# Optimization experiments

Hardware: AMD Instinct MI355X
Metric: run time of the kernel (lower is better)

The kernel has to match this reference:

```python
import jax, jax.numpy as jnp
import numpy as np

SHAPES = ((100, 152), (50, 76), (25, 38), (13, 19))  # per-level (H, W), stride 8/16/32/64 of 800x1216
S_TOTAL = sum(h * w for h, w in SHAPES)  # 20197
D, H, LVL, P, NL, H2 = 256, 8, 4, 4, 6, 2
B, NQ_TOTAL, NPROP = 8, 350, 300
DFF = 1024


def layer_norm(x, w, b, eps=1e-5):
    m = jnp.mean(x, -1, keepdims=True)
    v = jnp.mean((x - m) ** 2, -1, keepdims=True)
    return (x - m) / jnp.sqrt(v + eps) * w + b


def pos2posemb(pos, num_pos_feats=64, temperature=10000.0):
    pos = pos * (2.0 * np.pi)
    dim_t = temperature ** (2.0 * (jnp.arange(num_pos_feats) // 2).astype(jnp.float32) / num_pos_feats)
    pe = pos[..., None] / dim_t  # [..., 4, 64]
    pe = jnp.stack((jnp.sin(pe[..., 0::2]), jnp.cos(pe[..., 1::2])), axis=-1)  # [..., 4, 32, 2]
    return pe.reshape(pe.shape[:-3] + (-1,))  # [..., 256]


def bilinear_gather(v_l, loc, hl, wl):
    # v_l [B, hl*wl, H, Dh]; loc [B, Nq, H, P, 2] in [0,1]; grid_sample align_corners=False, zero padding
    b, nq, h, p, _ = loc.shape
    dh = v_l.shape[-1]
    x = loc[..., 0] * wl - 0.5
    y = loc[..., 1] * hl - 0.5
    x0 = jnp.floor(x)
    y0 = jnp.floor(y)
    lx = x - x0
    ly = y - y0

    def g(xi, yi):
        valid = (xi >= 0) & (xi <= wl - 1) & (yi >= 0) & (yi <= hl - 1)
        xi_i = jnp.clip(xi, 0, wl - 1).astype(jnp.int32)
        yi_i = jnp.clip(yi, 0, hl - 1).astype(jnp.int32)
        idx = (yi_i * wl + xi_i).transpose(0, 1, 3, 2).reshape(b, nq * p, h)  # per-head spatial index
        out = jnp.take_along_axis(v_l, jnp.broadcast_to(idx[..., None], (b, nq * p, h, dh)), axis=1)
        out = out.reshape(b, nq, p, h, dh).transpose(0, 1, 3, 2, 4)  # [B,Nq,H,P,Dh]
        return out * valid.astype(v_l.dtype)[..., None]

    return (g(x0, y0) * ((1 - lx) * (1 - ly))[..., None]
            + g(x0 + 1, y0) * (lx * (1 - ly))[..., None]
            + g(x0, y0 + 1) * ((1 - lx) * ly)[..., None]
            + g(x0 + 1, y0 + 1) * (lx * ly)[..., None])


def ms_deform_attn(query, ref, src, Woff, boff, Wa, ba, Wv, bv, Wout, bout):
    b, nq, d = query.shape
    dh = d // H
    value = (src @ Wv + bv).reshape(b, -1, H, dh)
    off = (query @ Woff + boff).reshape(b, nq, H, LVL, P, 2)
    attn = jax.nn.softmax((query @ Wa + ba).reshape(b, nq, H, LVL * P), -1).reshape(b, nq, H, LVL, P)
    # 4-d reference points: center + offsets scaled by box size
    loc = ref[:, :, None, :, None, :2] + off / P * ref[:, :, None, :, None, 2:] * 0.5  # [b,nq,H,L,P,2]
    out = jnp.zeros((b, nq, H, dh), query.dtype)
    start = 0
    for l, (hl, wl) in enumerate(SHAPES):
        v_l = value[:, start:start + hl * wl]
        start += hl * wl
        samp = bilinear_gather(v_l, loc[:, :, :, l], hl, wl)  # [b,nq,H,P,dh]
        out = out + (samp * attn[:, :, :, l, :, None]).sum(3)
    return out.reshape(b, nq, d) @ Wout + bout


def weight_attn(q_in, k_in, Wq, bq, Wk, bk):
    b, nq, d = q_in.shape
    nk = k_in.shape[1]
    dh = d // H2
    q = (q_in @ Wq + bq).reshape(b, nq, H2, dh).transpose(0, 2, 1, 3)
    k = (k_in @ Wk + bk).reshape(b, nk, H2, dh).transpose(0, 2, 1, 3)
    mm = jax.nn.softmax(jnp.einsum('bhqd,bhkd->bhqk', q, k) * (1.0 / dh ** 0.5), -1)
    qn = q / (jnp.linalg.norm(q, axis=-1, keepdims=True) + 1e-6)
    kn = k / (jnp.linalg.norm(k, axis=-1, keepdims=True) + 1e-6)
    cos = jnp.einsum('bhqd,bhkd->bhqk', qn, kn)
    return cos, mm


def setup_inputs():
    key = jax.random.key(0)
    ks = jax.random.split(key, 32)
    f = jnp.float32
    inp = {}
    inp['tgt'] = jax.random.normal(ks[0], (B, NQ_TOTAL, D), f)
    inp['reference_points'] = jax.random.uniform(ks[1], (B, NQ_TOTAL, 4), f, 0.05, 0.95)
    inp['src'] = jax.random.normal(ks[2], (B, S_TOTAL, D), f)
    inp['src_spatial_shapes'] = jnp.array(SHAPES, jnp.int32)
    lsi = np.cumsum([0] + [h * w for h, w in SHAPES])[:-1]
    inp['src_level_start_index'] = jnp.array(lsi, jnp.int32)
    inp['src_valid_ratios'] = jnp.ones((B, LVL, 2), f)
    inp['num_proposals'] = NPROP
    names = [('Woff', (NL, D, H * LVL * P * 2)), ('boff', (NL, H * LVL * P * 2)),
             ('Wa', (NL, D, H * LVL * P)), ('ba', (NL, H * LVL * P)),
             ('Wv', (NL, D, D)), ('bv', (NL, D)), ('Wout', (NL, D, D)), ('bout', (NL, D)),
             ('Wl1', (NL, D, DFF)), ('bl1', (NL, DFF)), ('Wl2', (NL, DFF, D)), ('bl2', (NL, D)),
             ('Wq', (NL, D, D)), ('bq', (NL, D)), ('Wk', (NL, D, D)), ('bk', (NL, D))]
    for i, (n, s) in enumerate(names):
        inp[n] = jax.random.normal(ks[3 + i], s, f) * 0.02
    inp['n1w'] = jnp.ones((NL, D), f)
    inp['n1b'] = jnp.zeros((NL, D), f)
    inp['n3w'] = jnp.ones((NL, D), f)
    inp['n3b'] = jnp.zeros((NL, D), f)
    return inp


def reference(tgt, reference_points, src, src_spatial_shapes, src_level_start_index,
              src_valid_ratios, num_proposals, Woff, boff, Wa, ba, Wv, bv, Wout, bout,
              Wl1, bl1, Wl2, bl2, Wq, bq, Wk, bk, n1w, n1b, n3w, n3b):
    proposals = tgt[:, :num_proposals]
    track_queries = tgt[:, num_proposals:]
    p_ref = reference_points[:, :num_proposals]
    t_ref = reference_points[:, num_proposals:]
    vr = jnp.concatenate([src_valid_ratios, src_valid_ratios], -1)  # [B,L,4]
    ref_input = p_ref[:, :, None] * vr[:, None]  # [B,Np,L,4]
    p_pos = pos2posemb(p_ref)
    t_pos = pos2posemb(t_ref)  # computed per torch code; WeightAttention ignores pos
    for l in range(NL):
        q = proposals + p_pos
        ca = ms_deform_attn(q, ref_input, src, Woff[l], boff[l], Wa[l], ba[l], Wv[l], bv[l], Wout[l], bout[l])
        proposals = layer_norm(proposals + ca, n1w[l], n1b[l])  # dropout = identity (eval)
        ffn = jax.nn.relu(proposals @ Wl1[l] + bl1[l]) @ Wl2[l] + bl2[l]
        proposals = layer_norm(proposals + ffn, n3w[l], n3b[l])
        pt_cos, pt_mm = weight_attn(proposals, track_queries, Wq[l], bq[l], Wk[l], bk[l])
        pp_cos, pp_mm = weight_attn(proposals, proposals, Wq[l], bq[l], Wk[l], bk[l])
    return proposals, p_ref, pt_cos, pp_cos, pt_mm, pp_mm
```

## Files before the change

### kernel.cpp

```cpp
#include <hip/hip_runtime.h>

#define BB 8
#define NQ 300
#define NTQ 50
#define NLAY 6
#define S_TOTAL 20197
#define ROWS (BB*NQ)
#define MVAL (BB*S_TOTAL)

typedef unsigned short u16;
typedef unsigned int u32;
typedef __bf16 v8bf __attribute__((ext_vector_type(8)));
typedef float f32x4 __attribute__((ext_vector_type(4)));

__device__ __forceinline__ u16 f2b(float f) {
    u32 u = __float_as_uint(f);
    u32 r = (u + 0x7fffu + ((u >> 16) & 1u)) >> 16;
    return (u16)r;
}
__device__ __forceinline__ u32 pk2(float lo, float hi) {
    return (u32)f2b(lo) | ((u32)f2b(hi) << 16);
}

#define ASYNC_CP16(dst_lds, src_g) \
    __builtin_amdgcn_global_load_lds((const __attribute__((address_space(1))) u32*)(src_g), \
                                     (__attribute__((address_space(3))) u32*)(dst_lds), 16, 0, 0)

__global__ void transpose_pack(
    const float* Woff, const float* Wa, const float* Wv, const float* Wout,
    const float* Wl1, const float* Wl2, const float* Wq, const float* Wk,
    const float* boff, const float* ba, const float* bvp, const float* bout,
    const float* bl1, const float* bl2, const float* bq, const float* bk,
    u16* wt, float* bias)
{
    int idx = blockIdx.x * 256 + threadIdx.x;
    if (idx < 5308416) {
        int l = idx / 884736;
        int o = idx % 884736;
        float v;
        if (o < 98304) { int n = o >> 8, k = o & 255;
            v = (n < 256) ? Woff[l*65536 + k*256 + n] : Wa[l*32768 + k*128 + (n-256)];
        } else if (o < 163840) { int o2 = o - 98304; int n = o2 >> 8, k = o2 & 255;
            v = Wv[l*65536 + k*256 + n];
        } else if (o < 229376) { int o2 = o - 163840; int n = o2 >> 8, k = o2 & 255;
            v = Wout[l*65536 + k*256 + n];
        } else if (o < 491520) { int o2 = o - 229376; int n = o2 >> 8, k = o2 & 255;
            v = Wl1[l*262144 + k*1024 + n];
        } else if (o < 753664) { int o2 = o - 491520; int n = o2 >> 10, k = o2 & 1023;
            v = Wl2[l*262144 + k*256 + n];
        } else { int o2 = o - 753664; int n = o2 >> 8, k = o2 & 255;
            v = (n < 256) ? Wq[l*65536 + k*256 + n] : Wk[l*65536 + k*256 + (n-256)];
        }
        wt[idx] = f2b(v);
    } else {
        int i2 = idx - 5308416;
        if (i2 < 16128) {
            int l = i2 / 2688, o = i2 % 2688;
            float v;
            if (o < 256)       v = boff[l*256 + o];
            else if (o < 384)  v = ba  [l*128 + (o-256)];
            else if (o < 640)  v = bvp [l*256 + (o-384)];
            else if (o < 896)  v = bout[l*256 + (o-640)];
            else if (o < 1920) v = bl1 [l*1024 + (o-896)];
            else if (o < 2176) v = bl2 [l*256 + (o-1920)];
            else if (o < 2432) v = bq  [l*256 + (o-2176)];
            else               v = bk  [l*256 + (o-2432)];
            bias[i2] = v;
        }
    }
}

__global__ void src_convert(const float* __restrict__ src, u16* __restrict__ dst)
{
    long i = ((long)blockIdx.x*256 + threadIdx.x)*8;
    float4 a = *(const float4*)(src+i), b4 = *(const float4*)(src+i+4);
    uint4 o = make_uint4(pk2(a.x,a.y), pk2(a.z,a.w), pk2(b4.x,b4.y), pk2(b4.z,b4.w));
    *(uint4*)&dst[i] = o;
}

__global__ void setup_kernel(const float* tgt, const float* refp, float* prop,
                             u16* q_b, float* ppos, u16* tq, float* out_pref)
{
    int row = blockIdx.x, t = threadIdx.x;
    if (row < ROWS) {
        int b = row / NQ, q = row % NQ;
        int k = t >> 6, rem = t & 63, j = rem >> 1;
        float pr = refp[(b*350 + q)*4 + k];
        float dimt = powf(10000.0f, (float)j * (1.0f/32.0f));
        float arg = pr * 6.283185307179586f / dimt;
        float pe = (rem & 1) ? cosf(arg) : sinf(arg);
        ppos[row*256 + t] = pe;
        float pv = tgt[(b*350 + q)*256 + t];
        prop[row*256 + t] = pv;
        q_b[row*256 + t] = f2b(pv + pe);
        if (t < 4) out_pref[row*4 + t] = refp[(b*350 + q)*4 + t];
    } else {
        int r2 = row - ROWS;
        int b = r2 / NTQ, qq = r2 % NTQ;
        tq[r2*256 + t] = f2b(tgt[(b*350 + NQ + qq)*256 + t]);
    }
}

__global__ __launch_bounds__(256) void gemm_bt64(
    const u16* __restrict__ A, const u16* __restrict__ Bt,
    const float* __restrict__ bias, void* __restrict__ Cout,
    int M, int N, int K, int flags)
{
    __shared__ __align__(16) u16 As[2][64*32];
    __shared__ __align__(16) u16 Bs[2][128*32];
    int tid = threadIdx.x;
    int lane = tid & 63, wave = tid >> 6;
    int bm = blockIdx.y * 64, bn = blockIdx.x * 128;
    int wm = (wave >> 1) * 32, wn = (wave & 1) * 64;
    f32x4 acc[2][4] = {};
    int r = tid >> 2, c = (tid & 3) * 8;
    const u16* Ap0 = A  + (long)min(bm + r,      M-1) * K + c;
    const u16* Bp0 = Bt + (long)min(bn + r,      N-1) * K + c;
    const u16* Bp1 = Bt + (long)min(bn + r + 64, N-1) * K + c;
    int fr = lane & 15, fk = (lane >> 4) * 8;

    auto STG = [&](int bi, int k0) {
        ASYNC_CP16(&As[bi][tid*8],         Ap0 + k0);
        ASYNC_CP16(&Bs[bi][tid*8],         Bp0 + k0);
        ASYNC_CP16(&Bs[bi][64*32 + tid*8], Bp1 + k0);
    };
    STG(0, 0);
    asm volatile("s_waitcnt vmcnt(0)" ::: "memory");
    __syncthreads();
    int cur = 0;
    for (int k0 = 0; k0 < K; k0 += 32) {
        if (k0 + 32 < K) STG(cur ^ 1, k0 + 32);
        v8bf af[2], bf[4];
        #pragma unroll
        for (int i = 0; i < 2; ++i) af[i] = *(const v8bf*)&As[cur][(wm + i*16 + fr)*32 + fk];
        #pragma unroll
        for (int j = 0; j < 4; ++j) bf[j] = *(const v8bf*)&Bs[cur][(wn + j*16 + fr)*32 + fk];
        #pragma unroll
        for (int i = 0; i < 2; ++i)
            #pragma unroll
            for (int j = 0; j < 4; ++j)
                acc[i][j] = __builtin_amdgcn_mfma_f32_16x16x32_bf16(af[i], bf[j], acc[i][j], 0, 0, 0);
        asm volatile("s_waitcnt vmcnt(0)" ::: "memory");
        __syncthreads();
        cur ^= 1;
    }
    int cq = lane >> 4, cn = lane & 15;
    #pragma unroll
    for (int i = 0; i < 2; ++i) {
        #pragma unroll
        for (int j = 0; j < 4; ++j) {
            int col = bn + wn + j*16 + cn;
            float bv_ = bias ? bias[col] : 0.0f;
            #pragma unroll
            for (int rr = 0; rr < 4; ++rr) {
                int m = bm + wm + i*16 + cq*4 + rr;
                if (m < M) {
                    float v = acc[i][j][rr] + bv_;
                    if (flags & 1) v = fmaxf(v, 0.0f);
                    if (flags & 2) ((u16*)Cout)[(long)m*N + col] = f2b(v);
                    else           ((float*)Cout)[(long)m*N + col] = v;
                }
            }
        }
    }
}

__global__ __launch_bounds__(256, 2) void gemm_value6_v3(
    const u16* __restrict__ A, const u16* __restrict__ wtall,
    const float* __restrict__ biasall, u16* __restrict__ Cout)
{
    __shared__ __align__(16) u16 Asw[8*4*128*8];
    __shared__ __align__(16) u16 Bsw[2][4*128*8];
    int tid = threadIdx.x;
    int lane = tid & 63, wave = tid >> 6;
    int fr = lane & 15, q = lane >> 4;
    int wm = (wave >> 1) * 64, wn = (wave & 1) * 64;
    long rowb = (long)blockIdx.x * 128;

    #pragma unroll
    for (int it = 0; it < 16; ++it) {
        int c_id = it*256 + tid;
        int row   = c_id & 127;
        int chunk = (c_id >> 7) & 3;
        int ks    = c_id >> 9;
        const u16* srcp = A + (long)min(rowb + row, (long)(MVAL-1))*256 + ks*32 + chunk*8;
        ASYNC_CP16(&Asw[(size_t)c_id*8], srcp);
    }
    {
        #pragma unroll
        for (int it = 0; it < 2; ++it) {
            int c_id = it*256 + tid;
            int col   = c_id & 127;
            int chunk = c_id >> 7;
            const u16* srcp = wtall + 98304 + (size_t)col*256 + chunk*8;
            ASYNC_CP16(&Bsw[0][(size_t)c_id*8], srcp);
        }
    }
    asm volatile("s_waitcnt vmcnt(0)" ::: "memory");
    __syncthreads();

    int buf = 0;
    for (int t = 0; t < 12; ++t) {
        int z = t >> 1, half = t & 1;
        u16* Cz = Cout + (size_t)z*((size_t)MVAL*256);
        const float* bs = biasall + z*2688 + 384 + half*128;
        float bc0 = bs[wn + fr], bc1 = bs[wn + 16 + fr],
              bc2 = bs[wn + 32 + fr], bc3 = bs[wn + 48 + fr];
        f32x4 acc[4][4] = {};
        #pragma unroll
        for (int ks = 0; ks < 8; ++ks) {
            int s = t*8 + ks;
            if (s < 95) {
                int sn = s + 1;
                int zn = sn >> 4, halfn = (sn >> 3) & 1, ksn = sn & 7;
                const u16* Bt = wtall + (size_t)zn*884736 + 98304;
                #pragma unroll
                for (int it = 0; it < 2; ++it) {
                    int c_id = it*256 + tid;
                    int col   = c_id & 127;
                    int chunk = c_id >> 7;
                    const u16* srcp = Bt + (size_t)(halfn*128 + col)*256 + ksn*32 + chunk*8;
                    ASYNC_CP16(&Bsw[buf ^ 1][(size_t)c_id*8], srcp);
                }
            }
            v8bf af[4], bf[4];
            #pragma unroll
            for (int i = 0; i < 4; ++i)
                af[i] = *(const v8bf*)&Asw[ks*4096 + q*1024 + (wm + i*16 + fr)*8];
            #pragma unroll
            for (int j = 0; j < 4; ++j)
                bf[j] = *(const v8bf*)&Bsw[buf][q*1024 + (wn + j*16 + fr)*8];
            #pragma unroll
            for (int i = 0; i < 4; ++i)
                #pragma unroll
                for (int j = 0; j < 4; ++j)
                    acc[i][j] = __builtin_amdgcn_mfma_f32_16x16x32_bf16(af[i], bf[j], acc[i][j], 0, 0, 0);
            asm volatile("s_waitcnt vmcnt(0)" ::: "memory");
            __syncthreads();
            buf ^= 1;
        }
        #pragma unroll
        for (int j = 0; j < 4; ++j) {
            int col = half*128 + wn + j*16 + fr;
            float bv_ = (j == 0) ? bc0 : (j == 1) ? bc1 : (j == 2) ? bc2 : bc3;
            #pragma unroll
            for (int rr = 0; rr < 4; ++rr) {
                long m = rowb + wm + q*4 + rr;
                long m1 = m + 16;
                (void)m1;
                #pragma unroll
                for (int i = 0; i < 4; ++i) {
                    long mi = rowb + wm + i*16 + q*4 + rr;
                    if (mi < MVAL) Cz[mi*256 + col] = f2b(acc[i][j][rr] + bv_);
                }
            }
        }
    }
}

__global__ __launch_bounds__(256) void sample_fused(
    const u16* __restrict__ value, const float* __restrict__ offatt,
    const float* __restrict__ refp, const float* __restrict__ svr,
    u16* __restrict__ sampout)
{
    int row = blockIdx.x, t = threadIdx.x;
    int b = row / NQ, q = row % NQ;
    __shared__ float lg[128], awl[128], sxl[128], syl[128];
    const int WL[4] = {152,76,38,19}, HL[4] = {100,50,25,13}, LS[4] = {0,15200,19000,19950};

    if (t < 128) lg[t] = offatt[row*384 + 256 + t];
    __syncthreads();
    if (t < 128) {
        int h = t >> 4, s = t & 15, lvl = s >> 2, pp = s & 3;
        int gb = h << 4;
        float mx = -1e30f;
        for (int i = 0; i < 16; ++i) mx = fmaxf(mx, lg[gb + i]);
        float sm = 0.f;
        for (int i = 0; i < 16; ++i) sm += expf(lg[gb + i] - mx);
        awl[t] = expf(lg[t] - mx) / sm;
        float rx = refp[(b*350+q)*4 + 0] * svr[(b*4+lvl)*2 + 0];
        float ry = refp[(b*350+q)*4 + 1] * svr[(b*4+lvl)*2 + 1];
        float rw = refp[(b*350+q)*4 + 2] * svr[(b*4+lvl)*2 + 0];
        float rh = refp[(b*350+q)*4 + 3] * svr[(b*4+lvl)*2 + 1];
        float ox = offatt[row*384 + h*32 + lvl*8 + pp*2 + 0];
        float oy = offatt[row*384 + h*32 + lvl*8 + pp*2 + 1];
        sxl[t] = (rx + ox * 0.25f * rw * 0.5f) * (float)WL[lvl] - 0.5f;
        syl[t] = (ry + oy * 0.25f * rh * 0.5f) * (float)HL[lvl] - 0.5f;
    }
    __syncthreads();

    int lane = t & 63, wv = t >> 6;
    int g = lane >> 3, e = lane & 7;
    for (int hh = 0; hh < 2; ++hh) {
        int h = wv*2 + hh;
        float a0 = 0.f, a1 = 0.f, a2 = 0.f, a3 = 0.f;
        #pragma unroll
        for (int it = 0; it < 8; ++it) {
            int task = it*8 + g;
            int s = task >> 2, cc = task & 3;
            int cx = cc & 1, cy = cc >> 1;
            int lvl = s >> 2;
            float x = sxl[h*16 + s], y2 = syl[h*16 + s], aw = awl[h*16 + s];
            float x0 = floorf(x), y0 = floorf(y2);
            float xc = x0 + (float)cx, yc = y0 + (float)cy;
            int wl = WL[lvl], hl = HL[lvl];
            if (xc >= 0.f && xc <= (float)(wl-1) && yc >= 0.f && yc <= (float)(hl-1)) {
                float lx = x - x0, ly = y2 - y0;
                float wgt = aw * (cx ? lx : 1.f - lx) * (cy ? ly : 1.f - ly);
                long off = ((long)b*S_TOTAL + LS[lvl] + (int)yc*wl + (int)xc)*256 + h*32 + e*4;
                uint2 v = *(const uint2*)(value + off);
                a0 += wgt * __uint_as_float((v.x & 0xffffu) << 16);
                a1 += wgt * __uint_as_float(v.x & 0xffff0000u);
                a2 += wgt * __uint_as_float((v.y & 0xffffu) << 16);
                a3 += wgt * __uint_as_float(v.y & 0xffff0000u);
            }
        }
        #pragma unroll
        for (int o = 8; o < 64; o <<= 1) {
            a0 += __shfl_xor(a0, o); a1 += __shfl_xor(a1, o);
            a2 += __shfl_xor(a2, o); a3 += __shfl_xor(a3, o);
        }
        if (g == 0)
            *(uint2*)&sampout[row*256 + h*32 + e*4] = make_uint2(pk2(a0, a1), pk2(a2, a3));
    }
}

__global__ void ln_kernel(float* __restrict__ prop, const float* __restrict__ delta,
                          const float* __restrict__ w, const float* __restrict__ bsh,
                          u16* __restrict__ pb_out, u16* __restrict__ q_out,
                          const float* __restrict__ ppos)
{
    int row = blockIdx.x, t = threadIdx.x;
    int lane = t & 63, wv = t >> 6;
    float v = prop[row*256 + t] + delta[row*256 + t];
    float s = v;
    for (int o = 32; o; o >>= 1) s += __shfl_xor(s, o);
    __shared__ float red[4], red2[4];
    if (lane == 0) red[wv] = s;
    __syncthreads();
    float mean = (red[0]+red[1]+red[2]+red[3]) * (1.0f/256.0f);
    float dd = v - mean;
    float s2 = dd * dd;
    for (int o = 32; o; o >>= 1) s2 += __shfl_xor(s2, o);
    if (lane == 0) red2[wv] = s2;
    __syncthreads();
    float var = (red2[0]+red2[1]+red2[2]+red2[3]) * (1.0f/256.0f);
    float nv = dd * rsqrtf(var + 1e-5f) * w[t] + bsh[t];
    prop[row*256 + t] = nv;
    pb_out[row*256 + t] = f2b(nv);
    if (q_out) q_out[row*256 + t] = f2b(nv + ppos[row*256 + t]);
}

__global__ __launch_bounds__(128) void qk_convert(
    const float* __restrict__ qkp, const float* __restrict__ kt,
    u16* __restrict__ qk_b, u16* __restrict__ kt_b,
    float* __restrict__ qn_g, float* __restrict__ knp_g, float* __restrict__ knt_g)
{
    int row = blockIdx.x, t = threadIdx.x;
    __shared__ float part[128];
    if (row < ROWS) {
        const float* sp = qkp + (long)row*512 + t*4;
        float4 v = *(const float4*)sp;
        *(uint2*)&qk_b[(long)row*512 + t*4] = make_uint2(pk2(v.x,v.y), pk2(v.z,v.w));
        part[t] = v.x*v.x + v.y*v.y + v.z*v.z + v.w*v.w;
        __syncthreads();
        if (t < 4) {
            float s = 0.f;
            for (int i = 0; i < 32; ++i) s += part[t*32 + i];
            int b = row / NQ, q = row % NQ;
            float nv = sqrtf(s) + 1e-6f;
            if      (t == 0) qn_g [(b*2+0)*NQ + q] = nv;
            else if (t == 1) qn_g [(b*2+1)*NQ + q] = nv;
            else if (t == 2) knp_g[(b*2+0)*NQ + q] = nv;
            else             knp_g[(b*2+1)*NQ + q] = nv;
        }
    } else {
        int r2 = row - ROWS;
        float ss = 0.f;
        if (t < 64) {
            const float* sp = kt + (long)r2*256 + t*4;
            float4 v = *(const float4*)sp;
            *(uint2*)&kt_b[(long)r2*256 + t*4] = make_uint2(pk2(v.x,v.y), pk2(v.z,v.w));
            ss = v.x*v.x + v.y*v.y + v.z*v.z + v.w*v.w;
        }
        part[t] = ss;
        __syncthreads();
        if (t < 2) {
            float s = 0.f;
            for (int i = 0; i < 32; ++i) s += part[t*32 + i];
            int b = r2 / NTQ, qq = r2 % NTQ;
            knt_g[(b*2+t)*NTQ + qq] = sqrtf(s) + 1e-6f;
        }
    }
}

__global__ __launch_bounds__(256) void wattn_mfma(
    const u16* __restrict__ Qb, const u16* __restrict__ Kb,
    int qstride, int kstride, int koff, int nk,
    const float* __restrict__ qn_g, const float* __restrict__ kn_g,
    float* __restrict__ out_cos, float* __restrict__ out_logit)
{
    __shared__ __align__(16) u16 As[2][128*32];
    __shared__ __align__(16) u16 Bs[2][128*32];
    int bh = blockIdx.z, b = bh >> 1, h = bh & 1;
    int tid = threadIdx.x;
    int lane = tid & 63, wave = tid >> 6;
    int bm = blockIdx.y * 128, bn = blockIdx.x * 128;
    int wm = (wave >> 1) * 64, wn = (wave & 1) * 64;
    f32x4 acc[4][4] = {};
    int r = tid >> 2, c = (tid & 3) * 8;
    const u16* Ap0 = Qb + (long)(b*NQ + min(bm + r,      NQ-1))*qstride + h*128 + c;
    const u16* Ap1 = Qb + (long)(b*NQ + min(bm + r + 64, NQ-1))*qstride + h*128 + c;
    const u16* Bp0 = Kb + (long)(b*nk + min(bn + r,      nk-1))*kstride + koff + h*128 + c;
    const u16* Bp1 = Kb + (long)(b*nk + min(bn + r + 64, nk-1))*kstride + koff + h*128 + c;
    int fr = lane & 15, fk = (lane >> 4) * 8;

    auto STG = [&](int bi, int k0) {
        ASYNC_CP16(&As[bi][tid*8],         Ap0 + k0);
        ASYNC_CP16(&As[bi][64*32 + tid*8], Ap1 + k0);
        ASYNC_CP16(&Bs[bi][tid*8],         Bp0 + k0);
        ASYNC_CP16(&Bs[bi][64*32 + tid*8], Bp1 + k0);
    };
    STG(0, 0);
    asm volatile("s_waitcnt vmcnt(0)" ::: "memory");
    __syncthreads();
    int cur = 0;
    for (int k0 = 0; k0 < 128; k0 += 32) {
        if (k0 + 32 < 128) STG(cur ^ 1, k0 + 32);
        v8bf af[4], bf[4];
        #pragma unroll
        for (int i = 0; i < 4; ++i) af[i] = *(const v8bf*)&As[cur][(wm + i*16 + fr)*32 + fk];
        #pragma unroll
        for (int j = 0; j < 4; ++j) bf[j] = *(const v8bf*)&Bs[cur][(wn + j*16 + fr)*32 + fk];
        #pragma unroll
        for (int i = 0; i < 4; ++i)
            #pragma unroll
            for (int j = 0; j < 4; ++j)
                acc[i][j] = __builtin_amdgcn_mfma_f32_16x16x32_bf16(af[i], bf[j], acc[i][j], 0, 0, 0);
        asm volatile("s_waitcnt vmcnt(0)" ::: "memory");
        __syncthreads();
        cur ^= 1;
    }
    const float SC = 0.08838834764831845f;
    int cq = lane >> 4, cn = lane & 15;
    #pragma unroll
    for (int i = 0; i < 4; ++i) {
        #pragma unroll
        for (int j = 0; j < 4; ++j) {
            int col = bn + wn + j*16 + cn;
            #pragma unroll
            for (int rr = 0; rr < 4; ++rr) {
                int m = bm + wm + i*16 + cq*4 + rr;
                if (m < NQ && col < nk) {
                    float d = acc[i][j][rr];
                    long o = ((long)(bh*NQ + m))*nk + col;
                    out_cos[o]   = d / (qn_g[bh*NQ + m] * kn_g[bh*nk + col]);
                    out_logit[o] = d * SC;
                }
            }
        }
    }
}

__global__ __launch_bounds__(64) void row_softmax(float* __restrict__ buf, int nk)
{
    long row = blockIdx.x;
    float* p = buf + row*nk;
    int lane = threadIdx.x;
    float mx = -1e30f;
    for (int k = lane; k < nk; k += 64) mx = fmaxf(mx, p[k]);
    for (int o = 32; o; o >>= 1) mx = fmaxf(mx, __shfl_xor(mx, o));
    float s = 0.f;
    for (int k = lane; k < nk; k += 64) s += expf(p[k] - mx);
    for (int o = 32; o; o >>= 1) s += __shfl_xor(s, o);
    float inv = 1.0f / s;
    for (int k = lane; k < nk; k += 64) p[k] = expf(p[k] - mx) * inv;
}

__global__ void writeout_kernel(const float* __restrict__ prop, float* __restrict__ out)
{
    int row = blockIdx.x, t = threadIdx.x;
    out[row*256 + t] = prop[row*256 + t];
}

extern "C" void kernel_launch(void* const* d_in, const int* in_sizes, int n_in,
                              void* d_out, int out_size, void* d_ws, size_t ws_size,
                              hipStream_t stream)
{
    (void)in_sizes; (void)n_in; (void)out_size; (void)ws_size;
    const float* tgt  = (const float*)d_in[0];
    const float* refp = (const float*)d_in[1];
    const float* src  = (const float*)d_in[2];
    const float* svr  = (const float*)d_in[5];
    const float* Woff = (const float*)d_in[7];
    const float* boff = (const float*)d_in[8];
    const float* Wa   = (const float*)d_in[9];
    const float* ba   = (const float*)d_in[10];
    const float* Wv   = (const float*)d_in[11];
    const float* bv   = (const float*)d_in[12];
    const float* Wout = (const float*)d_in[13];
    const float* bout = (const float*)d_in[14];
    const float* Wl1  = (const float*)d_in[15];
    const float* bl1  = (const float*)d_in[16];
    const float* Wl2  = (const float*)d_in[17];
    const float* bl2  = (const float*)d_in[18];
    const float* Wq   = (const float*)d_in[19];
    const float* bq   = (const float*)d_in[20];
    const float* Wk   = (const float*)d_in[21];
    const float* bk   = (const float*)d_in[22];
    const float* n1w  = (const float*)d_in[23];
    const float* n1b  = (const float*)d_in[24];
    const float* n3w  = (const float*)d_in[25];
    const float* n3b  = (const float*)d_in[26];
    float* out = (float*)d_out;

    char* p = (char*)d_ws;
    auto alloc = [&](size_t bytes) { void* r = (void*)p; p += (bytes + 255) & ~(size_t)255; return r; };
    u16*   wt      = (u16*)  alloc(6ull*884736*2);
    float* bias    = (float*)alloc(6ull*2688*4);
    u16*   value   = (u16*)  alloc(6ull*MVAL*256*2);
    u16*   src_b   = (u16*)  alloc((size_t)MVAL*256*2);
    float* prop    = (float*)alloc((size_t)ROWS*256*4);
    u16*   prop_b  = (u16*)  alloc((size_t)ROWS*256*2);
    u16*   q_b     = (u16*)  alloc((size_t)ROWS*256*2);
    float* ppos    = (float*)alloc((size_t)ROWS*256*4);
    float* offatt  = (float*)alloc((size_t)ROWS*384*4);
    u16*   sampout = (u16*)  alloc((size_t)ROWS*256*2);
    float* ca      = (float*)alloc((size_t)ROWS*256*4);
    u16*   ff1     = (u16*)  alloc((size_t)ROWS*1024*2);
    float* ff2     = (float*)alloc((size_t)ROWS*256*4);
    u16*   tq      = (u16*)  alloc(400ull*256*2);
    float* qkp     = (float*)alloc((size_t)ROWS*512*4);
    float* kt      = (float*)alloc(400ull*256*4);
    u16*   qk_b    = (u16*)  alloc((size_t)ROWS*512*2);
    u16*   kt_b    = (u16*)  alloc(400ull*256*2);
    float* qn_g    = (float*)alloc(16ull*NQ*4);
    float* knp_g   = (float*)alloc(16ull*NQ*4);
    float* knt_g   = (float*)alloc(16ull*NTQ*4);

    transpose_pack<<<20799, 256, 0, stream>>>(Woff, Wa, Wv, Wout, Wl1, Wl2, Wq, Wk,
                                              boff, ba, bv, bout, bl1, bl2, bq, bk, wt, bias);
    src_convert<<<20197, 256, 0, stream>>>(src, src_b);
    setup_kernel<<<ROWS + 400, 256, 0, stream>>>(tgt, refp, prop, q_b, ppos, tq, out + 614400);
    gemm_value6_v3<<<1263, 256, 0, stream>>>(src_b, wt, bias, value);

    for (int l = 0; l < NLAY; ++l) {
        const u16* wl_ = wt + (size_t)l*884736;
        const float* bl_ = bias + l*2688;
        gemm_bt64<<<dim3(3, 38), 256, 0, stream>>>(q_b,    wl_,          bl_,        offatt, ROWS, 384, 256, 0);
        sample_fused<<<ROWS, 256, 0, stream>>>(value + (size_t)l*MVAL*256, offatt, refp, svr, sampout);
        gemm_bt64<<<dim3(2, 38), 256, 0, stream>>>(sampout, wl_ + 163840, bl_ + 640,  ca,    ROWS, 256, 256, 0);
        ln_kernel<<<ROWS, 256, 0, stream>>>(prop, ca, n1w + l*256, n1b + l*256, prop_b, (u16*)nullptr, ppos);
        gemm_bt64<<<dim3(8, 38), 256, 0, stream>>>(prop_b, wl_ + 229376, bl_ + 896,  ff1,   ROWS, 1024, 256, 3);
        gemm_bt64<<<dim3(2, 38), 256, 0, stream>>>(ff1,    wl_ + 491520, bl_ + 1920, ff2,   ROWS, 256, 1024, 0);
        ln_kernel<<<ROWS, 256, 0, stream>>>(prop, ff2, n3w + l*256, n3b + l*256, prop_b, q_b, ppos);
    }

    const u16* w5 = wt + 5ull*884736;
    const float* b5 = bias + 5*2688;
    gemm_bt64<<<dim3(4, 38), 256, 0, stream>>>(prop_b, w5 + 753664,         b5 + 2176,       qkp, ROWS, 512, 256, 0);
    gemm_bt64<<<dim3(2, 7),  256, 0, stream>>>(tq,     w5 + 753664 + 65536, b5 + 2176 + 256, kt,  400,  256, 256, 0);
    qk_convert<<<2800, 128, 0, stream>>>(qkp, kt, qk_b, kt_b, qn_g, knp_g, knt_g);
    wattn_mfma<<<dim3(1, 3, 16), 256, 0, stream>>>(qk_b, kt_b, 512, 256, 0,   NTQ, qn_g, knt_g,
                                                   out + 624000, out + 2304000);
    wattn_mfma<<<dim3(3, 3, 16), 256, 0, stream>>>(qk_b, qk_b, 512, 512, 256, NQ,  qn_g, knp_g,
                                                   out + 864000, out + 2544000);
    row_softmax<<<4800, 64, 0, stream>>>(out + 2304000, NTQ);
    row_softmax<<<4800, 64, 0, stream>>>(out + 2544000, NQ);
    writeout_kernel<<<ROWS, 256, 0, stream>>>(prop, out);
}
```

Baseline: 1.289 ms.

## Fuse src bf16 conversion into value GEMM with register-resident A fragments

Removes the separate src fp32-to-bf16 conversion kernel and its intermediate buffer. The value-projection GEMM now loads fp32 src rows directly, converts them in registers and keeps each wave's 32-row A tile resident across all 12 output tiles (6 layers × 2 halves). B fragments are read straight from global memory with no LDS staging or barriers. This saves a full read/write pass over the source and the sync overhead, but B loads are no longer shared through LDS and register pressure rises considerably.

Result: slower. 1.512 ms (+17.3%).

```diff
diff --git a/kernel.cpp b/kernel.cpp
--- a/kernel.cpp
+++ b/kernel.cpp
@@ -70,14 +70,6 @@
     }
 }
 
-__global__ void src_convert(const float* __restrict__ src, u16* __restrict__ dst)
-{
-    long i = ((long)blockIdx.x*256 + threadIdx.x)*8;
-    float4 a = *(const float4*)(src+i), b4 = *(const float4*)(src+i+4);
-    uint4 o = make_uint4(pk2(a.x,a.y), pk2(a.z,a.w), pk2(b4.x,b4.y), pk2(b4.z,b4.w));
-    *(uint4*)&dst[i] = o;
-}
-
 __global__ void setup_kernel(const float* tgt, const float* refp, float* prop,
                              u16* q_b, float* ppos, u16* tq, float* out_pref)
 {
@@ -165,94 +157,63 @@
     }
 }
 
-__global__ __launch_bounds__(256, 2) void gemm_value6_v3(
-    const u16* __restrict__ A, const u16* __restrict__ wtall,
+__global__ __launch_bounds__(256, 2) void gemm_value6_v4(
+    const float* __restrict__ srcf, const u16* __restrict__ wtall,
     const float* __restrict__ biasall, u16* __restrict__ Cout)
 {
-    __shared__ __align__(16) u16 Asw[8*4*128*8];
-    __shared__ __align__(16) u16 Bsw[2][4*128*8];
     int tid = threadIdx.x;
     int lane = tid & 63, wave = tid >> 6;
     int fr = lane & 15, q = lane >> 4;
-    int wm = (wave >> 1) * 64, wn = (wave & 1) * 64;
-    long rowb = (long)blockIdx.x * 128;
-
+    long rowb = (long)blockIdx.x * 128 + wave*32;
+
+    const float* Ar0 = srcf + (long)min(rowb + fr,      (long)(MVAL-1))*256 + q*8;
+    const float* Ar1 = srcf + (long)min(rowb + 16 + fr, (long)(MVAL-1))*256 + q*8;
+    v8bf a0[8], a1[8];
     #pragma unroll
-    for (int it = 0; it < 16; ++it) {
-        int c_id = it*256 + tid;
-        int row   = c_id & 127;
-        int chunk = (c_id >> 7) & 3;
-        int ks    = c_id >> 9;
-        const u16* srcp = A + (long)min(rowb + row, (long)(MVAL-1))*256 + ks*32 + chunk*8;
-        ASYNC_CP16(&Asw[(size_t)c_id*8], srcp);
-    }
-    {
-        #pragma unroll
-        for (int it = 0; it < 2; ++it) {
-            int c_id = it*256 + tid;
-            int col   = c_id & 127;
-            int chunk = c_id >> 7;
-            const u16* srcp = wtall + 98304 + (size_t)col*256 + chunk*8;
-            ASYNC_CP16(&Bsw[0][(size_t)c_id*8], srcp);
-        }
-    }
-    asm volatile("s_waitcnt vmcnt(0)" ::: "memory");
-    __syncthreads();
-
-    int buf = 0;
+    for (int ks = 0; ks < 8; ++ks) {
+        float4 lo = *(const float4*)(Ar0 + ks*32);
+        float4 hi = *(const float4*)(Ar0 + ks*32 + 4);
+        uint4 pk = make_uint4(pk2(lo.x,lo.y), pk2(lo.z,lo.w), pk2(hi.x,hi.y), pk2(hi.z,hi.w));
+        a0[ks] = *(v8bf*)&pk;
+        float4 lo1 = *(const float4*)(Ar1 + ks*32);
+        float4 hi1 = *(const float4*)(Ar1 + ks*32 + 4);
+        uint4 pk1 = make_uint4(pk2(lo1.x,lo1.y), pk2(lo1.z,lo1.w), pk2(hi1.x,hi1.y), pk2(hi1.z,hi1.w));
+        a1[ks] = *(v8bf*)&pk1;
+    }
+
+    const u16* Bbase = wtall + 98304 + (size_t)fr*256 + q*8;
+
     for (int t = 0; t < 12; ++t) {
         int z = t >> 1, half = t & 1;
+        const u16* Bt = Bbase + (size_t)z*884736 + (size_t)(half*128)*256;
         u16* Cz = Cout + (size_t)z*((size_t)MVAL*256);
-        const float* bs = biasall + z*2688 + 384 + half*128;
-        float bc0 = bs[wn + fr], bc1 = bs[wn + 16 + fr],
-              bc2 = bs[wn + 32 + fr], bc3 = bs[wn + 48 + fr];
-        f32x4 acc[4][4] = {};
+        const float* bs = biasall + z*2688 + 384 + half*128 + fr;
+        float bc[8];
+        #pragma unroll
+        for (int j = 0; j < 8; ++j) bc[j] = bs[j*16];
+
+        f32x4 acc0[8] = {}, acc1[8] = {};
         #pragma unroll
         for (int ks = 0; ks < 8; ++ks) {
-            int s = t*8 + ks;
-            if (s < 95) {
-                int sn = s + 1;
-                int zn = sn >> 4, halfn = (sn >> 3) & 1, ksn = sn & 7;
-                const u16* Bt = wtall + (size_t)zn*884736 + 98304;
-                #pragma unroll
-                for (int it = 0; it < 2; ++it) {
-                    int c_id = it*256 + tid;
-                    int col   = c_id & 127;
-                    int chunk = c_id >> 7;
-                    const u16* srcp = Bt + (size_t)(halfn*128 + col)*256 + ksn*32 + chunk*8;
-                    ASYNC_CP16(&Bsw[buf ^ 1][(size_t)c_id*8], srcp);
-                }
+            v8bf bf[8];
+            #pragma unroll
+            for (int j = 0; j < 8; ++j)
+                bf[j] = *(const v8bf*)(Bt + (size_t)(j*16)*256 + ks*32);
+            #pragma unroll
+            for (int j = 0; j < 8; ++j) {
+                acc0[j] = __builtin_amdgcn_mfma_f32_16x16x32_bf16(a0[ks], bf[j], acc0[j], 0, 0, 0);
+                acc1[j] = __builtin_amdgcn_mfma_f32_16x16x32_bf16(a1[ks], bf[j], acc1[j], 0, 0, 0);
             }
-            v8bf af[4], bf[4];
-            #pragma unroll
-            for (int i = 0; i < 4; ++i)
-                af[i] = *(const v8bf*)&Asw[ks*4096 + q*1024 + (wm + i*16 + fr)*8];
-            #pragma unroll
-            for (int j = 0; j < 4; ++j)
-                bf[j] = *(const v8bf*)&Bsw[buf][q*1024 + (wn + j*16 + fr)*8];
-            #pragma unroll
-            for (int i = 0; i < 4; ++i)
-                #pragma unroll
-                for (int j = 0; j < 4; ++j)
-                    acc[i][j] = __builtin_amdgcn_mfma_f32_16x16x32_bf16(af[i], bf[j], acc[i][j], 0, 0, 0);
-            asm volatile("s_waitcnt vmcnt(0)" ::: "memory");
-            __syncthreads();
-            buf ^= 1;
-        }
-        #pragma unroll
-        for (int j = 0; j < 4; ++j) {
-            int col = half*128 + wn + j*16 + fr;
-            float bv_ = (j == 0) ? bc0 : (j == 1) ? bc1 : (j == 2) ? bc2 : bc3;
+        }
+        #pragma unroll
+        for (int j = 0; j < 8; ++j) {
+            int col = half*128 + j*16 + fr;
             #pragma unroll
             for (int rr = 0; rr < 4; ++rr) {
-                long m = rowb + wm + q*4 + rr;
-                long m1 = m + 16;
-                (void)m1;
-                #pragma unroll
-                for (int i = 0; i < 4; ++i) {
-                    long mi = rowb + wm + i*16 + q*4 + rr;
-                    if (mi < MVAL) Cz[mi*256 + col] = f2b(acc[i][j][rr] + bv_);
-                }
+                long m0 = rowb + q*4 + rr;
+                long m1 = rowb + 16 + q*4 + rr;
+                if (m0 < MVAL) Cz[m0*256 + col] = f2b(acc0[j][rr] + bc[j]);
+                if (m1 < MVAL) Cz[m1*256 + col] = f2b(acc1[j][rr] + bc[j]);
             }
         }
     }
@@ -519,7 +480,6 @@
     u16*   wt      = (u16*)  alloc(6ull*884736*2);
     float* bias    = (float*)alloc(6ull*2688*4);
     u16*   value   = (u16*)  alloc(6ull*MVAL*256*2);
-    u16*   src_b   = (u16*)  alloc((size_t)MVAL*256*2);
     float* prop    = (float*)alloc((size_t)ROWS*256*4);
     u16*   prop_b  = (u16*)  alloc((size_t)ROWS*256*2);
     u16*   q_b     = (u16*)  alloc((size_t)ROWS*256*2);
@@ -540,9 +500,8 @@
 
     transpose_pack<<<20799, 256, 0, stream>>>(Woff, Wa, Wv, Wout, Wl1, Wl2, Wq, Wk,
                                               boff, ba, bv, bout, bl1, bl2, bq, bk, wt, bias);
-    src_convert<<<20197, 256, 0, stream>>>(src, src_b);
     setup_kernel<<<ROWS + 400, 256, 0, stream>>>(tgt, refp, prop, q_b, ppos, tq, out + 614400);
-    gemm_value6_v3<<<1263, 256, 0, stream>>>(src_b, wt, bias, value);
+    gemm_value6_v4<<<1263, 256, 0, stream>>>(src, wt, bias, value);
 
     for (int l = 0; l < NLAY; ++l) {
         const u16* wl_ = wt + (size_t)l*884736;
```
